# Optimization experiments

Hardware: AMD Instinct MI355X
Metric: run time of the kernel (lower is better)

Reference implementation:

```python
import jax, jax.numpy as jnp
import numpy as np

B, N, F_IN, F_OUT = 4, 4096, 128, 128

def setup_inputs() -> dict:
    key = jax.random.key(0)
    k1, k2, k3 = jax.random.split(key, 3)
    x = jax.random.normal(k1, (B, N, F_IN), dtype=jnp.float32)
    adj = jax.random.uniform(k2, (B, N, N), dtype=jnp.float32)
    weight = jax.random.normal(k3, (F_IN, F_OUT), dtype=jnp.float32) * (6.0 / (F_IN + F_OUT)) ** 0.5
    bias = jnp.zeros((F_OUT,), dtype=jnp.float32)
    return {"x": x, "adj": adj, "weight": weight, "bias": bias}

def reference(x, adj, weight, bias):
    # Z = D^{-1/2} A D^{-1/2} X W + b   (activation=None)
    degree = jnp.sum(adj, axis=-1)                       # [B, N]
    d_inv = jnp.power(degree + 1e-6, -0.5)               # [B, N]
    # diag(d_inv) @ A @ diag(d_inv) == row/col elementwise scaling
    adj_norm = d_inv[:, :, None] * adj * d_inv[:, None, :]  # [B, N, N]
    z = jnp.einsum('bnm,bmf->bnf', adj_norm, x)          # [B, N, F_in]
    z = jnp.einsum('bnf,fo->bno', z, weight) + bias      # [B, N, F_out]
    return z
```

## Files before the change

### kernel.cpp

```cpp
#include <hip/hip_runtime.h>
#include <hip/hip_bf16.h>
#include <stdint.h>


#define NROW 4096
#define FDIM 128
#define NBATCH 4

typedef __bf16 bf16x8 __attribute__((ext_vector_type(8)));
typedef float f32x4 __attribute__((ext_vector_type(4)));

__global__ __launch_bounds__(256) void k_degree(const float* __restrict__ adj,
                                                float* __restrict__ dinv) {
  const int row = blockIdx.x * 4 + (threadIdx.x >> 6);
  const int lane = threadIdx.x & 63;
  const float4* arow = (const float4*)(adj + (size_t)row * NROW);
  float s = 0.f;
#pragma unroll
  for (int i = 0; i < 16; ++i) {
    float4 v = arow[lane + i * 64];
    s += (v.x + v.y) + (v.z + v.w);
  }
#pragma unroll
  for (int off = 32; off > 0; off >>= 1) s += __shfl_down(s, off, 64);
  if (lane == 0) dinv[row] = 1.0f / sqrtf(s + 1e-6f);
}

__global__ __launch_bounds__(256) void k_xst(const float* __restrict__ x,
                                             const float* __restrict__ dinv,
                                             __hip_bfloat16* __restrict__ xst) {
  const int bid = blockIdx.x;
  const int b = bid >> 7;
  const int m0 = (bid & 127) * 32;
  const int tid = threadIdx.x;
  __shared__ float tile[32 * 132];

  {
    const int ml = tid >> 3;
    const int fl = (tid & 7) * 16;
    const float dv = dinv[b * NROW + m0 + ml];
    const float* gx = x + ((size_t)b * NROW + m0 + ml) * FDIM + fl;
    float* dst = &tile[ml * 132 + fl];
#pragma unroll
    for (int j = 0; j < 16; j += 4) {
      float4 v = *(const float4*)(gx + j);
      v.x *= dv; v.y *= dv; v.z *= dv; v.w *= dv;
      *(float4*)(dst + j) = v;
    }
  }
  __syncthreads();
  {
    const int f = tid >> 1;
    const int mc = (tid & 1) * 16;
    union { __hip_bfloat16 h[16]; uint4 v[2]; } tmp;
#pragma unroll
    for (int j = 0; j < 16; ++j)
      tmp.h[j] = __float2bfloat16(tile[(mc + j) * 132 + f]);
    __hip_bfloat16* dst = xst + ((size_t)b * FDIM + f) * NROW + m0 + mc;
    *(uint4*)(dst) = tmp.v[0];
    *(uint4*)(dst + 8) = tmp.v[1];
  }
}

#define MT 32
#define KC 64
#define AS_ST 72
#define BS_ST 72
#define ZS_ST 136

__global__ __launch_bounds__(256, 2)
void k_gemm(const float* __restrict__ adj, const __hip_bfloat16* __restrict__ xst,
            const float* __restrict__ dinv, const float* __restrict__ w,
            const float* __restrict__ bias, float* __restrict__ out) {
  __shared__ union {
    struct { __hip_bfloat16 As[2][MT * AS_ST]; __hip_bfloat16 Bs[2][FDIM * BS_ST]; } lp;
    __hip_bfloat16 Zs[MT * ZS_ST];
  } sm;
  __shared__ float dinv_s[MT];

  const int bid = blockIdx.x;
  const int xcd = bid & 7;
  const int b = xcd >> 1;
  const int mtile = (bid >> 3) * 2 + (xcd & 1);
  const int row0 = mtile * MT;

  const int tid = threadIdx.x;
  const int lane = tid & 63;
  const int wid = tid >> 6;
  const int l16 = lane & 15;
  const int quad = lane >> 4;

  if (tid < MT) dinv_s[tid] = dinv[b * NROW + row0 + tid];

  const float* adj_b = adj + ((size_t)b * NROW + row0) * NROW;
  const __hip_bfloat16* xst_b = xst + (size_t)b * FDIM * NROW;

  f32x4 zero4;
  zero4.x = 0.f; zero4.y = 0.f; zero4.z = 0.f; zero4.w = 0.f;
  f32x4 acc[2][2];
#pragma unroll
  for (int rt = 0; rt < 2; ++rt)
#pragma unroll
    for (int ct = 0; ct < 2; ++ct) acc[rt][ct] = zero4;

  const int ar = tid >> 3;
  const int ac = (tid & 7) * 8;
  const int bfr = tid >> 1;
  const int bcc = (tid & 1) * 32;
  const float* ga = adj_b + (size_t)ar * NROW + ac;
  const __hip_bfloat16* gb = xst_b + (size_t)bfr * NROW + bcc;

  float4 pa0 = *(const float4*)(ga);
  float4 pa1 = *(const float4*)(ga + 4);
  uint4 pb0 = ((const uint4*)gb)[0];
  uint4 pb1 = ((const uint4*)gb)[1];
  uint4 pb2 = ((const uint4*)gb)[2];
  uint4 pb3 = ((const uint4*)gb)[3];

  int p = 0;
  for (int k0 = 0; k0 < NROW; k0 += KC) {
    {
      union { __hip_bfloat16 h[8]; uint4 u; } t;
      t.h[0] = __float2bfloat16(pa0.x); t.h[1] = __float2bfloat16(pa0.y);
      t.h[2] = __float2bfloat16(pa0.z); t.h[3] = __float2bfloat16(pa0.w);
      t.h[4] = __float2bfloat16(pa1.x); t.h[5] = __float2bfloat16(pa1.y);
      t.h[6] = __float2bfloat16(pa1.z); t.h[7] = __float2bfloat16(pa1.w);
      *(uint4*)&sm.lp.As[p][ar * AS_ST + ac] = t.u;
      __hip_bfloat16* q = &sm.lp.Bs[p][bfr * BS_ST + bcc];
      *(uint4*)(q) = pb0;
      *(uint4*)(q + 8) = pb1;
      *(uint4*)(q + 16) = pb2;
      *(uint4*)(q + 24) = pb3;
    }
    if (k0 + KC < NROW) {
      const float* gan = ga + k0 + KC;
      pa0 = *(const float4*)(gan);
      pa1 = *(const float4*)(gan + 4);
      const __hip_bfloat16* gbn = gb + k0 + KC;
      pb0 = ((const uint4*)gbn)[0];
      pb1 = ((const uint4*)gbn)[1];
      pb2 = ((const uint4*)gbn)[2];
      pb3 = ((const uint4*)gbn)[3];
    }
    __syncthreads();
#pragma unroll
    for (int kk = 0; kk < 2; ++kk) {
      bf16x8 af[2], bfv[2];
#pragma unroll
      for (int rt = 0; rt < 2; ++rt)
        af[rt] = *(const bf16x8*)&sm.lp.As[p][(rt * 16 + l16) * AS_ST + kk * 32 + quad * 8];
#pragma unroll
      for (int ct = 0; ct < 2; ++ct)
        bfv[ct] = *(const bf16x8*)&sm.lp.Bs[p][(wid * 32 + ct * 16 + l16) * BS_ST + kk * 32 + quad * 8];
#pragma unroll
      for (int rt = 0; rt < 2; ++rt)
#pragma unroll
        for (int ct = 0; ct < 2; ++ct)
          acc[rt][ct] = __builtin_amdgcn_mfma_f32_16x16x32_bf16(af[rt], bfv[ct], acc[rt][ct], 0, 0, 0);
    }
    p ^= 1;
  }
  __syncthreads();

#pragma unroll
  for (int rt = 0; rt < 2; ++rt)
#pragma unroll
    for (int ct = 0; ct < 2; ++ct)
#pragma unroll
      for (int i = 0; i < 4; ++i) {
        int r = rt * 16 + quad * 4 + i;
        int c = wid * 32 + ct * 16 + l16;
        sm.Zs[r * ZS_ST + c] = __float2bfloat16(acc[rt][ct][i] * dinv_s[r]);
      }
  __syncthreads();

  f32x4 acc2[2][2];
#pragma unroll
  for (int rt = 0; rt < 2; ++rt)
#pragma unroll
    for (int ct = 0; ct < 2; ++ct) acc2[rt][ct] = zero4;
#pragma unroll
  for (int kk = 0; kk < 4; ++kk) {
    bf16x8 za[2], wb[2];
#pragma unroll
    for (int rt = 0; rt < 2; ++rt)
      za[rt] = *(const bf16x8*)&sm.Zs[(rt * 16 + l16) * ZS_ST + kk * 32 + quad * 8];
#pragma unroll
    for (int ct = 0; ct < 2; ++ct) {
      const int o = wid * 32 + ct * 16 + l16;
      const float* gw = w + (kk * 32 + quad * 8) * FDIM + o;
      union { __hip_bfloat16 h[8]; bf16x8 v; } tw;
#pragma unroll
      for (int j = 0; j < 8; ++j)
        tw.h[j] = __float2bfloat16(gw[j * FDIM]);
      wb[ct] = tw.v;
    }
#pragma unroll
    for (int rt = 0; rt < 2; ++rt)
#pragma unroll
      for (int ct = 0; ct < 2; ++ct)
        acc2[rt][ct] = __builtin_amdgcn_mfma_f32_16x16x32_bf16(za[rt], wb[ct], acc2[rt][ct], 0, 0, 0);
  }

  float bv[2];
  bv[0] = bias[wid * 32 + l16];
  bv[1] = bias[wid * 32 + 16 + l16];
  float* ob = out + ((size_t)b * NROW + row0) * FDIM;
#pragma unroll
  for (int rt = 0; rt < 2; ++rt)
#pragma unroll
    for (int ct = 0; ct < 2; ++ct)
#pragma unroll
      for (int i = 0; i < 4; ++i) {
        int r = rt * 16 + quad * 4 + i;
        int o = wid * 32 + ct * 16 + l16;
        ob[(size_t)r * FDIM + o] = acc2[rt][ct][i] + bv[ct];
      }
}

extern "C" void kernel_launch(void* const* d_in, const int* in_sizes, int n_in,
                              void* d_out, int out_size, void* d_ws, size_t ws_size,
                              hipStream_t stream) {
  const float* x    = (const float*)d_in[0];
  const float* adj  = (const float*)d_in[1];
  const float* w    = (const float*)d_in[2];
  const float* bias = (const float*)d_in[3];
  float* out = (float*)d_out;

  float* dinv = (float*)d_ws;
  __hip_bfloat16* xst =
      (__hip_bfloat16*)((char*)d_ws + (size_t)NBATCH * NROW * sizeof(float));

  k_degree<<<NBATCH * NROW / 4, 256, 0, stream>>>(adj, dinv);
  k_xst<<<512, 256, 0, stream>>>(x, dinv, xst);
  k_gemm<<<512, 256, 0, stream>>>(adj, xst, dinv, w, bias, out);
}
```

Measured before the change: 419.8 us.

## Fuse degree and x-scaling kernels; halve GEMM row tile for more blocks

The separate degree-reduction and x-scale/transpose kernels are merged into one prep kernel. Each block now computes the degrees for its own 32 rows and keeps them in shared memory, which removes one launch and the global dinv round trip. The main GEMM shrinks its row tile from 32 to 16 rows, launches twice as many blocks, and asks for 4 blocks per CU. It also drops the register-prefetch double buffering in favour of a simple load, sync, compute, sync loop. This trades latency hiding inside each block for more occupancy and parallelism, and doubles how often the bf16 x tile is re-read across blocks.

Result: slower. 473.2 us (+12.7%).

```diff
diff --git a/kernel.cpp b/kernel.cpp
--- a/kernel.cpp
+++ b/kernel.cpp
@@ -10,35 +10,43 @@
 typedef __bf16 bf16x8 __attribute__((ext_vector_type(8)));
 typedef float f32x4 __attribute__((ext_vector_type(4)));
 
-__global__ __launch_bounds__(256) void k_degree(const float* __restrict__ adj,
-                                                float* __restrict__ dinv) {
-  const int row = blockIdx.x * 4 + (threadIdx.x >> 6);
-  const int lane = threadIdx.x & 63;
-  const float4* arow = (const float4*)(adj + (size_t)row * NROW);
-  float s = 0.f;
-#pragma unroll
-  for (int i = 0; i < 16; ++i) {
-    float4 v = arow[lane + i * 64];
-    s += (v.x + v.y) + (v.z + v.w);
-  }
-#pragma unroll
-  for (int off = 32; off > 0; off >>= 1) s += __shfl_down(s, off, 64);
-  if (lane == 0) dinv[row] = 1.0f / sqrtf(s + 1e-6f);
-}
-
-__global__ __launch_bounds__(256) void k_xst(const float* __restrict__ x,
-                                             const float* __restrict__ dinv,
-                                             __hip_bfloat16* __restrict__ xst) {
+__global__ __launch_bounds__(256) void k_prep(const float* __restrict__ adj,
+                                              const float* __restrict__ x,
+                                              float* __restrict__ dinv,
+                                              __hip_bfloat16* __restrict__ xst) {
   const int bid = blockIdx.x;
   const int b = bid >> 7;
   const int m0 = (bid & 127) * 32;
   const int tid = threadIdx.x;
+  const int lane = tid & 63;
+  const int wid = tid >> 6;
+
   __shared__ float tile[32 * 132];
+  __shared__ float dinv_l[32];
+
+  for (int r = 0; r < 8; ++r) {
+    const int row = m0 + wid * 8 + r;
+    const float4* arow = (const float4*)(adj + ((size_t)b * NROW + row) * NROW);
+    float s = 0.f;
+#pragma unroll
+    for (int i = 0; i < 16; ++i) {
+      float4 v = arow[lane + i * 64];
+      s += (v.x + v.y) + (v.z + v.w);
+    }
+#pragma unroll
+    for (int off = 32; off > 0; off >>= 1) s += __shfl_down(s, off, 64);
+    if (lane == 0) {
+      float dv = 1.0f / sqrtf(s + 1e-6f);
+      dinv_l[wid * 8 + r] = dv;
+      dinv[b * NROW + row] = dv;
+    }
+  }
+  __syncthreads();
 
   {
     const int ml = tid >> 3;
     const int fl = (tid & 7) * 16;
-    const float dv = dinv[b * NROW + m0 + ml];
+    const float dv = dinv_l[ml];
     const float* gx = x + ((size_t)b * NROW + m0 + ml) * FDIM + fl;
     float* dst = &tile[ml * 132 + fl];
 #pragma unroll
@@ -62,18 +70,18 @@
   }
 }
 
-#define MT 32
+#define MT 16
 #define KC 64
 #define AS_ST 72
 #define BS_ST 72
 #define ZS_ST 136
 
-__global__ __launch_bounds__(256, 2)
+__global__ __launch_bounds__(256, 4)
 void k_gemm(const float* __restrict__ adj, const __hip_bfloat16* __restrict__ xst,
             const float* __restrict__ dinv, const float* __restrict__ w,
             const float* __restrict__ bias, float* __restrict__ out) {
   __shared__ union {
-    struct { __hip_bfloat16 As[2][MT * AS_ST]; __hip_bfloat16 Bs[2][FDIM * BS_ST]; } lp;
+    struct { __hip_bfloat16 As[MT * AS_ST]; __hip_bfloat16 Bs[FDIM * BS_ST]; } lp;
     __hip_bfloat16 Zs[MT * ZS_ST];
   } sm;
   __shared__ float dinv_s[MT];
@@ -97,94 +105,67 @@
 
   f32x4 zero4;
   zero4.x = 0.f; zero4.y = 0.f; zero4.z = 0.f; zero4.w = 0.f;
-  f32x4 acc[2][2];
-#pragma unroll
-  for (int rt = 0; rt < 2; ++rt)
-#pragma unroll
-    for (int ct = 0; ct < 2; ++ct) acc[rt][ct] = zero4;
-
-  const int ar = tid >> 3;
-  const int ac = (tid & 7) * 8;
+  f32x4 acc[2];
+  acc[0] = zero4; acc[1] = zero4;
+
+  const int ar = tid >> 4;
+  const int ac = (tid & 15) * 4;
   const int bfr = tid >> 1;
   const int bcc = (tid & 1) * 32;
   const float* ga = adj_b + (size_t)ar * NROW + ac;
   const __hip_bfloat16* gb = xst_b + (size_t)bfr * NROW + bcc;
 
-  float4 pa0 = *(const float4*)(ga);
-  float4 pa1 = *(const float4*)(ga + 4);
-  uint4 pb0 = ((const uint4*)gb)[0];
-  uint4 pb1 = ((const uint4*)gb)[1];
-  uint4 pb2 = ((const uint4*)gb)[2];
-  uint4 pb3 = ((const uint4*)gb)[3];
-
-  int p = 0;
   for (int k0 = 0; k0 < NROW; k0 += KC) {
     {
-      union { __hip_bfloat16 h[8]; uint4 u; } t;
-      t.h[0] = __float2bfloat16(pa0.x); t.h[1] = __float2bfloat16(pa0.y);
-      t.h[2] = __float2bfloat16(pa0.z); t.h[3] = __float2bfloat16(pa0.w);
-      t.h[4] = __float2bfloat16(pa1.x); t.h[5] = __float2bfloat16(pa1.y);
-      t.h[6] = __float2bfloat16(pa1.z); t.h[7] = __float2bfloat16(pa1.w);
-      *(uint4*)&sm.lp.As[p][ar * AS_ST + ac] = t.u;
-      __hip_bfloat16* q = &sm.lp.Bs[p][bfr * BS_ST + bcc];
-      *(uint4*)(q) = pb0;
-      *(uint4*)(q + 8) = pb1;
-      *(uint4*)(q + 16) = pb2;
-      *(uint4*)(q + 24) = pb3;
-    }
-    if (k0 + KC < NROW) {
-      const float* gan = ga + k0 + KC;
-      pa0 = *(const float4*)(gan);
-      pa1 = *(const float4*)(gan + 4);
-      const __hip_bfloat16* gbn = gb + k0 + KC;
-      pb0 = ((const uint4*)gbn)[0];
-      pb1 = ((const uint4*)gbn)[1];
-      pb2 = ((const uint4*)gbn)[2];
-      pb3 = ((const uint4*)gbn)[3];
+      float4 v = *(const float4*)(ga + k0);
+      union { __hip_bfloat16 h[4]; uint2 u; } t;
+      t.h[0] = __float2bfloat16(v.x); t.h[1] = __float2bfloat16(v.y);
+      t.h[2] = __float2bfloat16(v.z); t.h[3] = __float2bfloat16(v.w);
+      *(uint2*)&sm.lp.As[ar * AS_ST + ac] = t.u;
+    }
+    {
+      const __hip_bfloat16* p = gb + k0;
+      uint4 u0 = ((const uint4*)p)[0];
+      uint4 u1 = ((const uint4*)p)[1];
+      uint4 u2 = ((const uint4*)p)[2];
+      uint4 u3 = ((const uint4*)p)[3];
+      __hip_bfloat16* q = &sm.lp.Bs[bfr * BS_ST + bcc];
+      *(uint4*)(q) = u0;
+      *(uint4*)(q + 8) = u1;
+      *(uint4*)(q + 16) = u2;
+      *(uint4*)(q + 24) = u3;
     }
     __syncthreads();
 #pragma unroll
     for (int kk = 0; kk < 2; ++kk) {
-      bf16x8 af[2], bfv[2];
-#pragma unroll
-      for (int rt = 0; rt < 2; ++rt)
-        af[rt] = *(const bf16x8*)&sm.lp.As[p][(rt * 16 + l16) * AS_ST + kk * 32 + quad * 8];
+      bf16x8 af = *(const bf16x8*)&sm.lp.As[l16 * AS_ST + kk * 32 + quad * 8];
+      bf16x8 bfv[2];
 #pragma unroll
       for (int ct = 0; ct < 2; ++ct)
-        bfv[ct] = *(const bf16x8*)&sm.lp.Bs[p][(wid * 32 + ct * 16 + l16) * BS_ST + kk * 32 + quad * 8];
-#pragma unroll
-      for (int rt = 0; rt < 2; ++rt)
-#pragma unroll
-        for (int ct = 0; ct < 2; ++ct)
-          acc[rt][ct] = __builtin_amdgcn_mfma_f32_16x16x32_bf16(af[rt], bfv[ct], acc[rt][ct], 0, 0, 0);
-    }
-    p ^= 1;
-  }
+        bfv[ct] = *(const bf16x8*)&sm.lp.Bs[(wid * 32 + ct * 16 + l16) * BS_ST + kk * 32 + quad * 8];
+#pragma unroll
+      for (int ct = 0; ct < 2; ++ct)
+        acc[ct] = __builtin_amdgcn_mfma_f32_16x16x32_bf16(af, bfv[ct], acc[ct], 0, 0, 0);
+    }
+    __syncthreads();
+  }
+
+#pragma unroll
+  for (int ct = 0; ct < 2; ++ct)
+#pragma unroll
+    for (int i = 0; i < 4; ++i) {
+      int r = quad * 4 + i;
+      int c = wid * 32 + ct * 16 + l16;
+      sm.Zs[r * ZS_ST + c] = __float2bfloat16(acc[ct][i] * dinv_s[r]);
+    }
   __syncthreads();
 
-#pragma unroll
-  for (int rt = 0; rt < 2; ++rt)
-#pragma unroll
-    for (int ct = 0; ct < 2; ++ct)
-#pragma unroll
-      for (int i = 0; i < 4; ++i) {
-        int r = rt * 16 + quad * 4 + i;
-        int c = wid * 32 + ct * 16 + l16;
-        sm.Zs[r * ZS_ST + c] = __float2bfloat16(acc[rt][ct][i] * dinv_s[r]);
-      }
-  __syncthreads();
-
-  f32x4 acc2[2][2];
-#pragma unroll
-  for (int rt = 0; rt < 2; ++rt)
-#pragma unroll
-    for (int ct = 0; ct < 2; ++ct) acc2[rt][ct] = zero4;
+  f32x4 acc2[2];
+  acc2[0] = zero4; acc2[1] = zero4;
 #pragma unroll
   for (int kk = 0; kk < 4; ++kk) {
-    bf16x8 za[2], wb[2];
-#pragma unroll
-    for (int rt = 0; rt < 2; ++rt)
-      za[rt] = *(const bf16x8*)&sm.Zs[(rt * 16 + l16) * ZS_ST + kk * 32 + quad * 8];
+    bf16x8 za = *(const bf16x8*)&sm.Zs[l16 * ZS_ST + kk * 32 + quad * 8];
+    bf16x8 wb[2];
 #pragma unroll
     for (int ct = 0; ct < 2; ++ct) {
       const int o = wid * 32 + ct * 16 + l16;
@@ -196,10 +177,8 @@
       wb[ct] = tw.v;
     }
 #pragma unroll
-    for (int rt = 0; rt < 2; ++rt)
-#pragma unroll
-      for (int ct = 0; ct < 2; ++ct)
-        acc2[rt][ct] = __builtin_amdgcn_mfma_f32_16x16x32_bf16(za[rt], wb[ct], acc2[rt][ct], 0, 0, 0);
+    for (int ct = 0; ct < 2; ++ct)
+      acc2[ct] = __builtin_amdgcn_mfma_f32_16x16x32_bf16(za, wb[ct], acc2[ct], 0, 0, 0);
   }
 
   float bv[2];
@@ -207,15 +186,13 @@
   bv[1] = bias[wid * 32 + 16 + l16];
   float* ob = out + ((size_t)b * NROW + row0) * FDIM;
 #pragma unroll
-  for (int rt = 0; rt < 2; ++rt)
-#pragma unroll
-    for (int ct = 0; ct < 2; ++ct)
-#pragma unroll
-      for (int i = 0; i < 4; ++i) {
-        int r = rt * 16 + quad * 4 + i;
-        int o = wid * 32 + ct * 16 + l16;
-        ob[(size_t)r * FDIM + o] = acc2[rt][ct][i] + bv[ct];
-      }
+  for (int ct = 0; ct < 2; ++ct)
+#pragma unroll
+    for (int i = 0; i < 4; ++i) {
+      int r = quad * 4 + i;
+      int o = wid * 32 + ct * 16 + l16;
+      ob[(size_t)r * FDIM + o] = acc2[ct][i] + bv[ct];
+    }
 }
 
 extern "C" void kernel_launch(void* const* d_in, const int* in_sizes, int n_in,
@@ -231,7 +208,6 @@
   __hip_bfloat16* xst =
       (__hip_bfloat16*)((char*)d_ws + (size_t)NBATCH * NROW * sizeof(float));
 
-  k_degree<<<NBATCH * NROW / 4, 256, 0, stream>>>(adj, dinv);
-  k_xst<<<512, 256, 0, stream>>>(x, dinv, xst);
-  k_gemm<<<512, 256, 0, stream>>>(adj, xst, dinv, w, bias, out);
+  k_prep<<<512, 256, 0, stream>>>(adj, x, dinv, xst);
+  k_gemm<<<1024, 256, 0, stream>>>(adj, xst, dinv, w, bias, out);
 }
```

## Replace double-buffered register prefetch with single-buffered larger K chunk

Applied to the files above, without the earlier changes.

The GEMM main loop drops the double-buffered LDS plus register prefetch and uses a single buffer with a K chunk of 128 instead of 64. Each iteration now loads, converts and stores directly, then computes, with two barriers per chunk. This halves the loop trip count and cuts LDS usage, but global loads are no longer overlapped with MFMA work except through occupancy across blocks.

After: 453.8 us. +8.1%, slower.

```diff
diff --git a/kernel.cpp b/kernel.cpp
--- a/kernel.cpp
+++ b/kernel.cpp
@@ -63,18 +63,16 @@
 }
 
 #define MT 32
-#define KC 64
-#define AS_ST 72
-#define BS_ST 72
-#define ZS_ST 136
+#define KC 128
+#define LST 136
 
 __global__ __launch_bounds__(256, 2)
 void k_gemm(const float* __restrict__ adj, const __hip_bfloat16* __restrict__ xst,
             const float* __restrict__ dinv, const float* __restrict__ w,
             const float* __restrict__ bias, float* __restrict__ out) {
   __shared__ union {
-    struct { __hip_bfloat16 As[2][MT * AS_ST]; __hip_bfloat16 Bs[2][FDIM * BS_ST]; } lp;
-    __hip_bfloat16 Zs[MT * ZS_ST];
+    struct { __hip_bfloat16 As[MT * LST]; __hip_bfloat16 Bs[FDIM * LST]; } lp;
+    __hip_bfloat16 Zs[MT * LST];
   } sm;
   __shared__ float dinv_s[MT];
 
@@ -104,63 +102,56 @@
     for (int ct = 0; ct < 2; ++ct) acc[rt][ct] = zero4;
 
   const int ar = tid >> 3;
-  const int ac = (tid & 7) * 8;
+  const int ac = (tid & 7) * 16;
   const int bfr = tid >> 1;
-  const int bcc = (tid & 1) * 32;
+  const int bcc = (tid & 1) * 64;
   const float* ga = adj_b + (size_t)ar * NROW + ac;
   const __hip_bfloat16* gb = xst_b + (size_t)bfr * NROW + bcc;
 
-  float4 pa0 = *(const float4*)(ga);
-  float4 pa1 = *(const float4*)(ga + 4);
-  uint4 pb0 = ((const uint4*)gb)[0];
-  uint4 pb1 = ((const uint4*)gb)[1];
-  uint4 pb2 = ((const uint4*)gb)[2];
-  uint4 pb3 = ((const uint4*)gb)[3];
-
-  int p = 0;
   for (int k0 = 0; k0 < NROW; k0 += KC) {
     {
-      union { __hip_bfloat16 h[8]; uint4 u; } t;
-      t.h[0] = __float2bfloat16(pa0.x); t.h[1] = __float2bfloat16(pa0.y);
-      t.h[2] = __float2bfloat16(pa0.z); t.h[3] = __float2bfloat16(pa0.w);
-      t.h[4] = __float2bfloat16(pa1.x); t.h[5] = __float2bfloat16(pa1.y);
-      t.h[6] = __float2bfloat16(pa1.z); t.h[7] = __float2bfloat16(pa1.w);
-      *(uint4*)&sm.lp.As[p][ar * AS_ST + ac] = t.u;
-      __hip_bfloat16* q = &sm.lp.Bs[p][bfr * BS_ST + bcc];
-      *(uint4*)(q) = pb0;
-      *(uint4*)(q + 8) = pb1;
-      *(uint4*)(q + 16) = pb2;
-      *(uint4*)(q + 24) = pb3;
-    }
-    if (k0 + KC < NROW) {
-      const float* gan = ga + k0 + KC;
-      pa0 = *(const float4*)(gan);
-      pa1 = *(const float4*)(gan + 4);
-      const __hip_bfloat16* gbn = gb + k0 + KC;
-      pb0 = ((const uint4*)gbn)[0];
-      pb1 = ((const uint4*)gbn)[1];
-      pb2 = ((const uint4*)gbn)[2];
-      pb3 = ((const uint4*)gbn)[3];
+      const float4* p = (const float4*)(ga + k0);
+      float4 v0 = p[0], v1 = p[1], v2 = p[2], v3 = p[3];
+      union { __hip_bfloat16 h[16]; uint4 u[2]; } t;
+      t.h[0] = __float2bfloat16(v0.x);  t.h[1] = __float2bfloat16(v0.y);
+      t.h[2] = __float2bfloat16(v0.z);  t.h[3] = __float2bfloat16(v0.w);
+      t.h[4] = __float2bfloat16(v1.x);  t.h[5] = __float2bfloat16(v1.y);
+      t.h[6] = __float2bfloat16(v1.z);  t.h[7] = __float2bfloat16(v1.w);
+      t.h[8] = __float2bfloat16(v2.x);  t.h[9] = __float2bfloat16(v2.y);
+      t.h[10] = __float2bfloat16(v2.z); t.h[11] = __float2bfloat16(v2.w);
+      t.h[12] = __float2bfloat16(v3.x); t.h[13] = __float2bfloat16(v3.y);
+      t.h[14] = __float2bfloat16(v3.z); t.h[15] = __float2bfloat16(v3.w);
+      uint4* q = (uint4*)&sm.lp.As[ar * LST + ac];
+      q[0] = t.u[0];
+      q[1] = t.u[1];
+    }
+    {
+      const uint4* p = (const uint4*)(gb + k0);
+      uint4 u[8];
+#pragma unroll
+      for (int j = 0; j < 8; ++j) u[j] = p[j];
+      uint4* q = (uint4*)&sm.lp.Bs[bfr * LST + bcc];
+#pragma unroll
+      for (int j = 0; j < 8; ++j) q[j] = u[j];
     }
     __syncthreads();
 #pragma unroll
-    for (int kk = 0; kk < 2; ++kk) {
+    for (int kk = 0; kk < 4; ++kk) {
       bf16x8 af[2], bfv[2];
 #pragma unroll
       for (int rt = 0; rt < 2; ++rt)
-        af[rt] = *(const bf16x8*)&sm.lp.As[p][(rt * 16 + l16) * AS_ST + kk * 32 + quad * 8];
+        af[rt] = *(const bf16x8*)&sm.lp.As[(rt * 16 + l16) * LST + kk * 32 + quad * 8];
 #pragma unroll
       for (int ct = 0; ct < 2; ++ct)
-        bfv[ct] = *(const bf16x8*)&sm.lp.Bs[p][(wid * 32 + ct * 16 + l16) * BS_ST + kk * 32 + quad * 8];
+        bfv[ct] = *(const bf16x8*)&sm.lp.Bs[(wid * 32 + ct * 16 + l16) * LST + kk * 32 + quad * 8];
 #pragma unroll
       for (int rt = 0; rt < 2; ++rt)
 #pragma unroll
         for (int ct = 0; ct < 2; ++ct)
           acc[rt][ct] = __builtin_amdgcn_mfma_f32_16x16x32_bf16(af[rt], bfv[ct], acc[rt][ct], 0, 0, 0);
     }
-    p ^= 1;
-  }
-  __syncthreads();
+    __syncthreads();
+  }
 
 #pragma unroll
   for (int rt = 0; rt < 2; ++rt)
@@ -170,7 +161,7 @@
       for (int i = 0; i < 4; ++i) {
         int r = rt * 16 + quad * 4 + i;
         int c = wid * 32 + ct * 16 + l16;
-        sm.Zs[r * ZS_ST + c] = __float2bfloat16(acc[rt][ct][i] * dinv_s[r]);
+        sm.Zs[r * LST + c] = __float2bfloat16(acc[rt][ct][i] * dinv_s[r]);
       }
   __syncthreads();
 
@@ -184,7 +175,7 @@
     bf16x8 za[2], wb[2];
 #pragma unroll
     for (int rt = 0; rt < 2; ++rt)
-      za[rt] = *(const bf16x8*)&sm.Zs[(rt * 16 + l16) * ZS_ST + kk * 32 + quad * 8];
+      za[rt] = *(const bf16x8*)&sm.Zs[(rt * 16 + l16) * LST + kk * 32 + quad * 8];
 #pragma unroll
     for (int ct = 0; ct < 2; ++ct) {
       const int o = wid * 32 + ct * 16 + l16;
```
